# Optimization experiments

Measured on AMD Instinct MI355X. Metric: run time of the kernel, lower is better.

Reference implementation:

```python
import jax, jax.numpy as jnp
import numpy as np

B, A, H, W = 16, 3, 80, 80
NUM_CLASSES = 80
C = 4 + NUM_CLASSES  # box(4) + [obj-as-class0 + remaining classes]
N_TGT = 64


def setup_inputs() -> dict:
    key = jax.random.key(0)
    pred = jax.random.normal(key, (B, A, H, W, C), dtype=jnp.float32)
    # Build targets with DISTINCT, SORTED grid cells so that the original
    # module's boolean-mask gather order pairs cell k with target k.
    rng = np.random.default_rng(0)
    cells = np.sort(rng.choice(H * W, size=N_TGT, replace=False))
    gy, gx = cells // W, cells % W
    cls_id = rng.integers(0, NUM_CLASSES, size=N_TGT).astype(np.float32)
    wh = (rng.random((N_TGT, 2)) * 0.2 + 0.02).astype(np.float32)
    targets = np.stack(
        [cls_id, (gx + 0.5) / W, (gy + 0.5) / H, wh[:, 0], wh[:, 1]], axis=1
    ).astype(np.float32)  # [N,5] = (class, x, y, w, h)
    return {"pred": pred, "targets": jnp.asarray(targets)}


def reference(pred, targets):
    Bs, As, Hs, Ws, Cs = pred.shape
    hw = Hs * Ws
    # grid assignment: (x*W, y*H) floored and clamped, like .long().clamp_
    gx = jnp.clip(jnp.floor(targets[:, 1] * Ws), 0, Ws - 1).astype(jnp.int32)
    gy = jnp.clip(jnp.floor(targets[:, 2] * Hs), 0, Hs - 1).astype(jnp.int32)
    cells = gy * Ws + gx  # [N]

    pf = pred.reshape(Bs, As, hw, Cs)
    pc = pf[:, :, cells, :]  # gather object cells -> [B, A, N, C]

    # loc: MSE of predicted box vs target (x,y,w,h), tiled over B*A
    boxes = targets[:, 1:5]  # [N,4]
    loc_loss = jnp.mean((pc[..., :4] - boxes) ** 2)

    # cls: BCEWithLogits of pred[...,4:] vs one-hot(class) over C-4 channels
    onehot = jax.nn.one_hot(targets[:, 0].astype(jnp.int32), Cs - 4, dtype=pred.dtype)
    logits = pc[..., 4:]  # [B,A,N,C-4]
    cls_loss = jnp.mean(jax.nn.softplus(logits) - logits * onehot)

    # obj: BCEWithLogits(pred[...,4][obj_mask], 1) = softplus(-logit)
    obj_loss = jnp.mean(jax.nn.softplus(-pc[..., 4]))

    # noobj: BCEWithLogits(pred[...,4][~obj_mask], 0) = softplus(logit)
    sp = jax.nn.softplus(pf[..., 4])  # [B,A,HW]
    cell_mask = jnp.zeros(hw, pred.dtype).at[cells].set(1.0)  # unique object cells
    n_obj_cells = cell_mask.sum()
    noobj_count = Bs * As * (hw - n_obj_cells)
    noobj_loss = jnp.sum(sp * (1.0 - cell_mask)) / noobj_count

    obj_scale, noobj_scale = 1.0, 0.5
    total = loc_loss + cls_loss + obj_scale * obj_loss + noobj_scale * noobj_loss
    return total  # single prediction scale -> divide by 1
```

## Files before the change

kernel.cpp:

```cpp
#include <hip/hip_runtime.h>
#include <math.h>

constexpr int BDIM  = 256;
constexpr int Bsz   = 16, Asz = 3, Hsz = 80, Wsz = 80;
constexpr int Csz   = 84;
constexpr int HWsz  = Hsz * Wsz;
constexpr int BAsz  = Bsz * Asz;
constexpr int TOTAL = BAsz * HWsz;
constexpr int NTGT  = 64;
constexpr int NCOMBO = BAsz * NTGT;
constexpr int GITER = 8;
constexpr int GBLK  = TOTAL / (BDIM * GITER);
constexpr int TBLK  = BAsz;
constexpr int NBLK  = GBLK + TBLK;
constexpr int NSP   = GBLK * 4;
static_assert(GBLK * BDIM * GITER == TOTAL, "exact cover");

__device__ __forceinline__ float softplus_fast(float x) {
    return fmaxf(x, 0.f) + __logf(1.f + __expf(-fabsf(x)));
}

__global__ __launch_bounds__(BDIM)
void yolo_main(const float* __restrict__ pred,
               const float* __restrict__ targets,
               float* __restrict__ partial_sp,
               float* __restrict__ partial_tgt) {
    int lane = threadIdx.x & 63, wid = threadIdx.x >> 6;

    if (blockIdx.x < GBLK) {
        int base = blockIdx.x * (BDIM * GITER) + threadIdx.x;
        float v[GITER];
        #pragma unroll
        for (int k = 0; k < GITER; ++k) {
            v[k] = pred[(size_t)(base + k * BDIM) * Csz + 4];
        }
        float sp = 0.f;
        #pragma unroll
        for (int k = 0; k < GITER; ++k) sp += softplus_fast(v[k]);
        #pragma unroll
        for (int o = 32; o > 0; o >>= 1) sp += __shfl_down(sp, o, 64);
        if (lane == 0) partial_sp[blockIdx.x * 4 + wid] = sp;
        return;
    }

    __shared__ float smem[NTGT * 5];
    int ba = blockIdx.x - GBLK;
    for (int i = threadIdx.x; i < NTGT * 5; i += BDIM) smem[i] = targets[i];
    __syncthreads();

    const float* __restrict__ pb = pred + (size_t)ba * HWsz * Csz;
    float cls = 0.f, locv = 0.f, obj = 0.f, spt = 0.f;

    #pragma unroll 4
    for (int k = 0; k < NTGT / 4; ++k) {
        int t = wid * (NTGT / 4) + k;
        const float* tg = &smem[t * 5];
        float cid_f = tg[0];
        int gx = min(max((int)floorf(tg[1] * (float)Wsz), 0), Wsz - 1);
        int gy = min(max((int)floorf(tg[2] * (float)Hsz), 0), Hsz - 1);
        int cell = gy * Wsz + gx;
        const float* p = pb + (size_t)cell * Csz;
        int cid4 = 4 + (int)cid_f;

        float v0 = p[lane];
        if (lane < 4) {
            float d = v0 - tg[1 + lane];
            locv += d * d;
        } else {
            cls += softplus_fast(v0);
        }
        if (lane == 4) {
            obj += softplus_fast(-v0);
            spt += softplus_fast(v0);
        }
        if (lane == cid4) cls -= v0;
        if (lane < 20) {
            float v1 = p[64 + lane];
            cls += softplus_fast(v1);
            if (lane + 64 == cid4) cls -= v1;
        }
    }

    float vals[4] = {cls, locv, obj, spt};
    #pragma unroll
    for (int q = 0; q < 4; ++q) {
        float v = vals[q];
        #pragma unroll
        for (int o = 32; o > 0; o >>= 1) v += __shfl_down(v, o, 64);
        vals[q] = v;
    }
    __shared__ float rsm[4][4];
    if (lane == 0) {
        #pragma unroll
        for (int q = 0; q < 4; ++q) rsm[wid][q] = vals[q];
    }
    __syncthreads();
    if (threadIdx.x == 0) {
        #pragma unroll
        for (int q = 0; q < 4; ++q)
            partial_tgt[ba * 4 + q] = rsm[0][q] + rsm[1][q] + rsm[2][q] + rsm[3][q];
    }
}

__global__ __launch_bounds__(BDIM)
void yolo_final(const float* __restrict__ partial_sp,
                const float* __restrict__ partial_tgt,
                float* __restrict__ out) {
    int lane = threadIdx.x & 63, wid = threadIdx.x >> 6;
    float s[5] = {0.f, 0.f, 0.f, 0.f, 0.f};
    for (int i = threadIdx.x; i < NSP; i += BDIM) s[0] += partial_sp[i];
    if (threadIdx.x < TBLK) {
        s[1] = partial_tgt[threadIdx.x * 4 + 0];
        s[2] = partial_tgt[threadIdx.x * 4 + 1];
        s[3] = partial_tgt[threadIdx.x * 4 + 2];
        s[4] = partial_tgt[threadIdx.x * 4 + 3];
    }
    #pragma unroll
    for (int q = 0; q < 5; ++q) {
        float v = s[q];
        #pragma unroll
        for (int o = 32; o > 0; o >>= 1) v += __shfl_down(v, o, 64);
        s[q] = v;
    }
    __shared__ float sm[4][5];
    if (lane == 0) {
        #pragma unroll
        for (int q = 0; q < 5; ++q) sm[wid][q] = s[q];
    }
    __syncthreads();
    if (threadIdx.x == 0) {
        float sp_all = sm[0][0] + sm[1][0] + sm[2][0] + sm[3][0];
        float cls    = sm[0][1] + sm[1][1] + sm[2][1] + sm[3][1];
        float loc    = sm[0][2] + sm[1][2] + sm[2][2] + sm[3][2];
        float obj    = sm[0][3] + sm[1][3] + sm[2][3] + sm[3][3];
        float spt    = sm[0][4] + sm[1][4] + sm[2][4] + sm[3][4];
        float loc_loss = loc / (float)(NCOMBO * 4);
        float cls_loss = cls / (float)(NCOMBO * 80);
        float obj_loss = obj / (float)NCOMBO;
        float noobj    = (sp_all - spt) / (float)(BAsz * (HWsz - NTGT));
        out[0] = loc_loss + cls_loss + obj_loss + 0.5f * noobj;
    }
}

extern "C" void kernel_launch(void* const* d_in, const int* in_sizes, int n_in,
                              void* d_out, int out_size, void* d_ws, size_t ws_size,
                              hipStream_t stream) {
    const float* pred    = (const float*)d_in[0];
    const float* targets = (const float*)d_in[1];
    float* partial_sp  = (float*)d_ws;
    float* partial_tgt = partial_sp + NSP;
    float* out = (float*)d_out;

    yolo_main<<<NBLK, BDIM, 0, stream>>>(pred, targets, partial_sp, partial_tgt);
    yolo_final<<<1, BDIM, 0, stream>>>(partial_sp, partial_tgt, out);
}
```

Measured before the change: 150.7 us.

## Fuse final reduction into main kernel via last-block atomic counter

Merges the two-kernel scheme into one kernel in which every block increments a global counter after writing its partials, and the last block to arrive does the final reduction. Partial slots are padded to 32 floats per block to keep them on separate cache lines. This removes a second kernel launch and its dependency gap, at the cost of a memset launch to reset the counter, an atomic per block and fences.

```diff
diff --git a/kernel.cpp b/kernel.cpp
--- a/kernel.cpp
+++ b/kernel.cpp
@@ -13,7 +13,7 @@
 constexpr int GBLK  = TOTAL / (BDIM * GITER);
 constexpr int TBLK  = BAsz;
 constexpr int NBLK  = GBLK + TBLK;
-constexpr int NSP   = GBLK * 4;
+constexpr int PAD   = 32;
 static_assert(GBLK * BDIM * GITER == TOTAL, "exact cover");
 
 __device__ __forceinline__ float softplus_fast(float x) {
@@ -21,99 +21,107 @@
 }
 
 __global__ __launch_bounds__(BDIM)
-void yolo_main(const float* __restrict__ pred,
-               const float* __restrict__ targets,
-               float* __restrict__ partial_sp,
-               float* __restrict__ partial_tgt) {
+void yolo_fused(const float* __restrict__ pred,
+                const float* __restrict__ targets,
+                float* __restrict__ ws_part,
+                unsigned int* __restrict__ counter,
+                float* __restrict__ out) {
+    float* sp_part  = ws_part;
+    float* tgt_part = ws_part + GBLK * PAD;
     int lane = threadIdx.x & 63, wid = threadIdx.x >> 6;
+    __shared__ float smem[NTGT * 5];
+    __shared__ float rsm[4][5];
+    __shared__ bool  amLast;
 
     if (blockIdx.x < GBLK) {
         int base = blockIdx.x * (BDIM * GITER) + threadIdx.x;
         float v[GITER];
         #pragma unroll
-        for (int k = 0; k < GITER; ++k) {
+        for (int k = 0; k < GITER; ++k)
             v[k] = pred[(size_t)(base + k * BDIM) * Csz + 4];
-        }
         float sp = 0.f;
         #pragma unroll
         for (int k = 0; k < GITER; ++k) sp += softplus_fast(v[k]);
         #pragma unroll
         for (int o = 32; o > 0; o >>= 1) sp += __shfl_down(sp, o, 64);
-        if (lane == 0) partial_sp[blockIdx.x * 4 + wid] = sp;
-        return;
-    }
+        if (lane == 0) sp_part[blockIdx.x * PAD + wid] = sp;
+    } else {
+        int ba = blockIdx.x - GBLK;
+        for (int i = threadIdx.x; i < NTGT * 5; i += BDIM) smem[i] = targets[i];
+        __syncthreads();
 
-    __shared__ float smem[NTGT * 5];
-    int ba = blockIdx.x - GBLK;
-    for (int i = threadIdx.x; i < NTGT * 5; i += BDIM) smem[i] = targets[i];
-    __syncthreads();
+        const float* __restrict__ pb = pred + (size_t)ba * HWsz * Csz;
+        float cls = 0.f, locv = 0.f, obj = 0.f, spt = 0.f;
 
-    const float* __restrict__ pb = pred + (size_t)ba * HWsz * Csz;
-    float cls = 0.f, locv = 0.f, obj = 0.f, spt = 0.f;
+        #pragma unroll 4
+        for (int k = 0; k < NTGT / 4; ++k) {
+            int t = wid * (NTGT / 4) + k;
+            const float* tg = &smem[t * 5];
+            float cid_f = tg[0];
+            int gx = min(max((int)floorf(tg[1] * (float)Wsz), 0), Wsz - 1);
+            int gy = min(max((int)floorf(tg[2] * (float)Hsz), 0), Hsz - 1);
+            int cell = gy * Wsz + gx;
+            const float* p = pb + (size_t)cell * Csz;
+            int cid4 = 4 + (int)cid_f;
 
-    #pragma unroll 4
-    for (int k = 0; k < NTGT / 4; ++k) {
-        int t = wid * (NTGT / 4) + k;
-        const float* tg = &smem[t * 5];
-        float cid_f = tg[0];
-        int gx = min(max((int)floorf(tg[1] * (float)Wsz), 0), Wsz - 1);
-        int gy = min(max((int)floorf(tg[2] * (float)Hsz), 0), Hsz - 1);
-        int cell = gy * Wsz + gx;
-        const float* p = pb + (size_t)cell * Csz;
-        int cid4 = 4 + (int)cid_f;
+            float v0 = p[lane];
+            if (lane < 4) {
+                float d = v0 - tg[1 + lane];
+                locv += d * d;
+            } else {
+                cls += softplus_fast(v0);
+            }
+            if (lane == 4) {
+                obj += softplus_fast(-v0);
+                spt += softplus_fast(v0);
+            }
+            if (lane == cid4) cls -= v0;
+            if (lane < 20) {
+                float v1 = p[64 + lane];
+                cls += softplus_fast(v1);
+                if (lane + 64 == cid4) cls -= v1;
+            }
+        }
 
-        float v0 = p[lane];
-        if (lane < 4) {
-            float d = v0 - tg[1 + lane];
-            locv += d * d;
-        } else {
-            cls += softplus_fast(v0);
+        float vals[4] = {cls, locv, obj, spt};
+        #pragma unroll
+        for (int q = 0; q < 4; ++q) {
+            float v = vals[q];
+            #pragma unroll
+            for (int o = 32; o > 0; o >>= 1) v += __shfl_down(v, o, 64);
+            vals[q] = v;
         }
-        if (lane == 4) {
-            obj += softplus_fast(-v0);
-            spt += softplus_fast(v0);
+        if (lane == 0) {
+            #pragma unroll
+            for (int q = 0; q < 4; ++q) rsm[wid][q] = vals[q];
         }
-        if (lane == cid4) cls -= v0;
-        if (lane < 20) {
-            float v1 = p[64 + lane];
-            cls += softplus_fast(v1);
-            if (lane + 64 == cid4) cls -= v1;
+        __syncthreads();
+        if (threadIdx.x == 0) {
+            #pragma unroll
+            for (int q = 0; q < 4; ++q)
+                tgt_part[ba * PAD + q] =
+                    rsm[0][q] + rsm[1][q] + rsm[2][q] + rsm[3][q];
         }
     }
 
-    float vals[4] = {cls, locv, obj, spt};
-    #pragma unroll
-    for (int q = 0; q < 4; ++q) {
-        float v = vals[q];
-        #pragma unroll
-        for (int o = 32; o > 0; o >>= 1) v += __shfl_down(v, o, 64);
-        vals[q] = v;
-    }
-    __shared__ float rsm[4][4];
-    if (lane == 0) {
-        #pragma unroll
-        for (int q = 0; q < 4; ++q) rsm[wid][q] = vals[q];
+    __syncthreads();
+    if (threadIdx.x == 0) {
+        __threadfence();
+        unsigned old = atomicAdd(counter, 1u);
+        amLast = (old == (unsigned)(NBLK - 1));
     }
     __syncthreads();
-    if (threadIdx.x == 0) {
-        #pragma unroll
-        for (int q = 0; q < 4; ++q)
-            partial_tgt[ba * 4 + q] = rsm[0][q] + rsm[1][q] + rsm[2][q] + rsm[3][q];
-    }
-}
+    if (!amLast) return;
 
-__global__ __launch_bounds__(BDIM)
-void yolo_final(const float* __restrict__ partial_sp,
-                const float* __restrict__ partial_tgt,
-                float* __restrict__ out) {
-    int lane = threadIdx.x & 63, wid = threadIdx.x >> 6;
+    __threadfence();
     float s[5] = {0.f, 0.f, 0.f, 0.f, 0.f};
-    for (int i = threadIdx.x; i < NSP; i += BDIM) s[0] += partial_sp[i];
+    for (int i = threadIdx.x; i < GBLK * 4; i += BDIM)
+        s[0] += sp_part[(i >> 2) * PAD + (i & 3)];
     if (threadIdx.x < TBLK) {
-        s[1] = partial_tgt[threadIdx.x * 4 + 0];
-        s[2] = partial_tgt[threadIdx.x * 4 + 1];
-        s[3] = partial_tgt[threadIdx.x * 4 + 2];
-        s[4] = partial_tgt[threadIdx.x * 4 + 3];
+        s[1] = tgt_part[threadIdx.x * PAD + 0];
+        s[2] = tgt_part[threadIdx.x * PAD + 1];
+        s[3] = tgt_part[threadIdx.x * PAD + 2];
+        s[4] = tgt_part[threadIdx.x * PAD + 3];
     }
     #pragma unroll
     for (int q = 0; q < 5; ++q) {
@@ -122,18 +130,18 @@
         for (int o = 32; o > 0; o >>= 1) v += __shfl_down(v, o, 64);
         s[q] = v;
     }
-    __shared__ float sm[4][5];
+    __syncthreads();
     if (lane == 0) {
         #pragma unroll
-        for (int q = 0; q < 5; ++q) sm[wid][q] = s[q];
+        for (int q = 0; q < 5; ++q) rsm[wid][q] = s[q];
     }
     __syncthreads();
     if (threadIdx.x == 0) {
-        float sp_all = sm[0][0] + sm[1][0] + sm[2][0] + sm[3][0];
-        float cls    = sm[0][1] + sm[1][1] + sm[2][1] + sm[3][1];
-        float loc    = sm[0][2] + sm[1][2] + sm[2][2] + sm[3][2];
-        float obj    = sm[0][3] + sm[1][3] + sm[2][3] + sm[3][3];
-        float spt    = sm[0][4] + sm[1][4] + sm[2][4] + sm[3][4];
+        float sp_all = rsm[0][0] + rsm[1][0] + rsm[2][0] + rsm[3][0];
+        float cls    = rsm[0][1] + rsm[1][1] + rsm[2][1] + rsm[3][1];
+        float loc    = rsm[0][2] + rsm[1][2] + rsm[2][2] + rsm[3][2];
+        float obj    = rsm[0][3] + rsm[1][3] + rsm[2][3] + rsm[3][3];
+        float spt    = rsm[0][4] + rsm[1][4] + rsm[2][4] + rsm[3][4];
         float loc_loss = loc / (float)(NCOMBO * 4);
         float cls_loss = cls / (float)(NCOMBO * 80);
         float obj_loss = obj / (float)NCOMBO;
@@ -147,10 +155,10 @@
                               hipStream_t stream) {
     const float* pred    = (const float*)d_in[0];
     const float* targets = (const float*)d_in[1];
-    float* partial_sp  = (float*)d_ws;
-    float* partial_tgt = partial_sp + NSP;
+    float* ws_part = (float*)d_ws;
+    unsigned int* counter = (unsigned int*)(ws_part + NBLK * PAD);
     float* out = (float*)d_out;
 
-    yolo_main<<<NBLK, BDIM, 0, stream>>>(pred, targets, partial_sp, partial_tgt);
-    yolo_final<<<1, BDIM, 0, stream>>>(partial_sp, partial_tgt, out);
+    hipMemsetAsync(counter, 0, sizeof(unsigned int), stream);
+    yolo_fused<<<NBLK, BDIM, 0, stream>>>(pred, targets, ws_part, counter, out);
 }
```

New measurement: 155.8 us. +3.4%, slower.
